# Optimization experiments

Hardware: AMD Instinct MI355X
Metric: run time of the kernel (lower is better)

## Reference

```python
import jax, jax.numpy as jnp
import numpy as np

MIN_, MAX_, KSZ, IGNORE_IDX = 10, 10, 3, -255
B, H, W = 256, 256, 256
LI_MAX_ITERS = 64


def setup_inputs() -> dict:
    key = jax.random.key(0)
    x = jax.random.uniform(key, (B, 1, H, W), dtype=jnp.float32)
    return {"x": x}


def _otsu(hist):
    # hist: [256] counts. Returns Otsu threshold (bin value); fg = img > t.
    bins = jnp.arange(256, dtype=jnp.float32)
    w0 = jnp.cumsum(hist)[:-1]
    w1 = hist.sum() - w0
    s0 = jnp.cumsum(hist * bins)[:-1]
    s_tot = (hist * bins).sum()
    m0 = s0 / jnp.maximum(w0, 1e-12)
    m1 = (s_tot - s0) / jnp.maximum(w1, 1e-12)
    var_b = w0 * w1 * (m0 - m1) ** 2
    return jnp.argmax(var_b).astype(jnp.float32)


def _li(hist, init_t):
    # Histogram-based Li iterative minimum cross-entropy threshold
    # (skimage.filters.threshold_li with initial_guess=init_t).
    bins = jnp.arange(256, dtype=jnp.float32)
    img_min = jnp.min(jnp.where(hist > 0, bins, 255.0))
    vals = bins - img_min  # shift so values >= 0 (as skimage does)
    csum = jnp.cumsum(hist)
    cvsum = jnp.cumsum(hist * vals)
    n_tot, s_tot = csum[-1], cvsum[-1]
    tol = 0.5  # integer image -> half the minimal value spacing

    def body(state):
        t_curr, _, i = state
        # background: img <= t_curr + img_min
        idx = jnp.clip(jnp.floor(t_curr + img_min).astype(jnp.int32), 0, 255)
        n_back, s_back = csum[idx], cvsum[idx]
        n_fore, s_fore = n_tot - n_back, s_tot - s_back
        mean_back = jnp.where(n_back > 0, s_back / jnp.maximum(n_back, 1.0), 0.0)
        mean_fore = s_fore / jnp.maximum(n_fore, 1.0)
        eps = 1e-12
        t_next = (mean_back - mean_fore) / (
            jnp.log(jnp.maximum(mean_back, eps)) - jnp.log(jnp.maximum(mean_fore, eps)))
        t_next = jnp.where(mean_back < eps, mean_fore / 2.0, t_next)
        return (t_next, t_curr, i + 1)

    def cond(state):
        t_curr, t_prev, i = state
        return (jnp.abs(t_curr - t_prev) > tol) & (i < LI_MAX_ITERS)

    t0 = init_t - img_min
    t_fin, _, _ = jax.lax.while_loop(cond, body, (t0, t0 + 10.0, 0))
    return t_fin + img_min


def _sample_mask(key, region, k):
    # Uniform sampling without replacement of up to k pixels from region
    # (bool [H,W]) via random-score top-k (equiv. to torch.multinomial
    # with uniform probs, w/o replacement).
    flat = region.reshape(-1)
    scores = jnp.where(flat, jax.random.uniform(key, (flat.shape[0],)), -1.0)
    top, idx = jax.lax.top_k(scores, k)
    valid = (top >= 0.0).astype(jnp.int32)
    mask = jnp.zeros(flat.shape[0], jnp.int32).at[idx].max(valid)
    return mask.reshape(region.shape)


def _dilate(m):
    # kornia dilation with ones (KSZ,KSZ) kernel on a 0/1 mask == max filter.
    return jax.lax.reduce_window(m, 0, jax.lax.max, (KSZ, KSZ), (1, 1), "SAME")


def _per_image(img_u8, key_fg, key_bg):
    # img_u8: [H,W] int32 in [0,255]
    hist = jnp.zeros(256, jnp.float32).at[img_u8.ravel()].add(1.0)
    otsu = jnp.clip(_otsu(hist), 1.0, 254.0)  # clamp 0->1, 255->254
    li_t = _li(hist, otsu)
    roi = img_u8.astype(jnp.float32) > li_t

    fg = _sample_mask(key_fg, roi, MAX_)
    bg = _sample_mask(key_bg, jnp.logical_not(roi), MIN_)
    if KSZ > 1:
        fg = _dilate(fg)
        bg = _dilate(bg)

    overlap = (fg + bg) == 2
    fg = jnp.where(overlap, 0, fg)
    bg = jnp.where(overlap, 0, bg)

    seeds = jnp.full((H, W), IGNORE_IDX, jnp.int32)
    seeds = jnp.where(bg == 1, 0, seeds)
    seeds = jnp.where(fg == 1, 1, seeds)
    return seeds


def reference(x):
    b = x.shape[0]
    # (cam*255).astype(uint8): truncation, cam in [0,1]
    img = jnp.clip(jnp.floor(x[:, 0] * 255.0), 0, 255).astype(jnp.int32)
    keys = jax.random.split(jax.random.key(1), (b, 2))
    return jax.vmap(_per_image)(img, keys[:, 0], keys[:, 1])
```

## Files before the change

kernel.cpp:

```cpp
#include <hip/hip_runtime.h>
#include <stdint.h>

#define NPIX 65536
#define IGN (-255)
#define CAPB 96

typedef unsigned long long u64;
typedef int v4i __attribute__((ext_vector_type(4)));

__device__ __forceinline__ uint32_t rotl32(uint32_t v, uint32_t r){ return (v<<r)|(v>>(32u-r)); }

__device__ __forceinline__ void tf2x32(uint32_t k0, uint32_t k1, uint32_t x0, uint32_t x1,
                                       uint32_t &o0, uint32_t &o1){
  uint32_t k2 = k0 ^ k1 ^ 0x1BD11BDAu;
  x0 += k0; x1 += k1;
#define TFR(r) { x0 += x1; x1 = rotl32(x1,(r)); x1 ^= x0; }
  TFR(13u) TFR(15u) TFR(26u) TFR(6u)   x0 += k1; x1 += k2 + 1u;
  TFR(17u) TFR(29u) TFR(16u) TFR(24u)  x0 += k2; x1 += k0 + 2u;
  TFR(13u) TFR(15u) TFR(26u) TFR(6u)   x0 += k0; x1 += k1 + 3u;
  TFR(17u) TFR(29u) TFR(16u) TFR(24u)  x0 += k1; x1 += k2 + 4u;
  TFR(13u) TFR(15u) TFR(26u) TFR(6u)   x0 += k2; x1 += k0 + 5u;
#undef TFR
  o0 = x0; o1 = x1;
}

__device__ __forceinline__ uint32_t tf_bits(uint32_t k0, uint32_t k1, uint32_t k2, uint32_t pix){
  uint32_t x0 = k0, x1 = pix + k1;
#define TFR(r) { x0 += x1; x1 = rotl32(x1,(r)); x1 ^= x0; }
  TFR(13u) TFR(15u) TFR(26u) TFR(6u)   x0 += k1; x1 += k2 + 1u;
  TFR(17u) TFR(29u) TFR(16u) TFR(24u)  x0 += k2; x1 += k0 + 2u;
  TFR(13u) TFR(15u) TFR(26u) TFR(6u)   x0 += k0; x1 += k1 + 3u;
  TFR(17u) TFR(29u) TFR(16u) TFR(24u)  x0 += k1; x1 += k2 + 4u;
  TFR(13u) TFR(15u) TFR(26u) TFR(6u)   x0 += k2; x1 += k0 + 5u;
#undef TFR
  return x0 ^ x1;
}

__device__ __forceinline__ u64 packCand(uint32_t bits, uint32_t pix){
  float f = __uint_as_float((bits >> 9) | 0x3f800000u) - 1.0f;
  uint32_t u = __float_as_uint(f) ^ 0x80000000u;
  return ((u64)u << 32) | (u64)(0xFFFFFFFFu - pix);
}

__device__ __forceinline__ void t10_insert(u64* l, u64 c){
  if (c > l[9]) {
    l[9] = c;
#pragma unroll
    for (int i = 9; i > 0; --i){
      u64 a = l[i-1], b2 = l[i];
      if (b2 > a){ l[i-1] = b2; l[i] = a; }
    }
  }
}

__global__ __launch_bounds__(256)
void k1_hist(const float* __restrict__ x, int* __restrict__ out,
             uint32_t* __restrict__ phist, uint32_t* __restrict__ u8c, int use_u8){
  const int img = blockIdx.x >> 3;
  const int chk = blockIdx.x & 7;
  const int tid = threadIdx.x;
  const float4* x4 = (const float4*)(x + (size_t)img * NPIX);
  v4i* o4 = (v4i*)(out + (size_t)img * NPIX);

  __shared__ uint32_t h4[1024];
  h4[tid] = 0u; h4[tid+256] = 0u; h4[tid+512] = 0u; h4[tid+768] = 0u;
  __syncthreads();

  const int sub = tid & 3;
  const v4i f4 = {IGN, IGN, IGN, IGN};
#pragma unroll
  for (int j = 0; j < 8; ++j){
    int p4 = chk*2048 + j*256 + tid;
    float4 v = x4[p4];
    __builtin_nontemporal_store(f4, &o4[p4]);
    uint32_t q0 = (uint32_t)min(max((int)floorf(v.x*255.0f),0),255);
    uint32_t q1 = (uint32_t)min(max((int)floorf(v.y*255.0f),0),255);
    uint32_t q2 = (uint32_t)min(max((int)floorf(v.z*255.0f),0),255);
    uint32_t q3 = (uint32_t)min(max((int)floorf(v.w*255.0f),0),255);
    if (use_u8) u8c[(size_t)img*16384 + p4] = q0 | (q1<<8) | (q2<<16) | (q3<<24);
    atomicAdd(&h4[q0*4+sub],1u); atomicAdd(&h4[q1*4+sub],1u);
    atomicAdd(&h4[q2*4+sub],1u); atomicAdd(&h4[q3*4+sub],1u);
  }
  __syncthreads();
  phist[(size_t)(img*8+chk)*256 + tid] = h4[tid*4] + h4[tid*4+1] + h4[tid*4+2] + h4[tid*4+3];
}

__global__ __launch_bounds__(256)
void k2_score(const float* __restrict__ x, const uint32_t* __restrict__ u8c,
              const uint32_t* __restrict__ phist, uint32_t* __restrict__ qcutp,
              uint32_t* __restrict__ nroip, uint32_t* __restrict__ bcnt,
              u64* __restrict__ cand, int use_u8){
  const int img = blockIdx.x >> 3;
  const int chk = blockIdx.x & 7;
  const int tid = threadIdx.x;

  __shared__ float csum[256], cvsum[256];
  __shared__ u64 s_best;
  __shared__ int s_imin, s_qcut;
  __shared__ uint32_t s_kw[4], s_cnt[2];
  __shared__ u64 s_cand[2][CAPB];

  if (tid < 2){
    uint32_t o0, o1;
    tf2x32(0u, 1u, 0u, (uint32_t)(2*img + tid), o0, o1);
    s_kw[2*tid] = o0; s_kw[2*tid+1] = o1;
  }
  if (tid == 0){ s_imin = 255; s_best = 0ull; s_cnt[0] = 0u; s_cnt[1] = 0u; }

  uint32_t h = 0;
#pragma unroll
  for (int k = 0; k < 8; ++k) h += phist[(size_t)(img*8+k)*256 + tid];
  __syncthreads();
  if (h) atomicMin(&s_imin, tid);
  __syncthreads();
  const float img_min = (float)s_imin;
  csum[tid]  = (float)h;
  cvsum[tid] = (float)h * ((float)tid - img_min);
  __syncthreads();
  for (int off = 1; off < 256; off <<= 1){
    float a = 0.f, c2 = 0.f;
    if (tid >= off){ a = csum[tid-off]; c2 = cvsum[tid-off]; }
    __syncthreads();
    if (tid >= off){ csum[tid] += a; cvsum[tid] += c2; }
    __syncthreads();
  }
  {
    float s_tot_o = cvsum[255] + img_min * csum[255];
    if (tid < 255){
      float w0 = csum[tid], w1 = 65536.0f - w0;
      float cs = cvsum[tid] + img_min * csum[tid];
      float m0 = cs / fmaxf(w0, 1e-12f);
      float m1 = (s_tot_o - cs) / fmaxf(w1, 1e-12f);
      float d = m0 - m1;
      float vb = (w0*w1) * (d*d);
      u64 pk = ((u64)__float_as_uint(vb) << 32) | (u64)(255 - tid);
      atomicMax(&s_best, pk);
    }
  }
  __syncthreads();
  if (tid == 0){
    int bestIdx = 255 - (int)(s_best & 0xFFFFFFFFull);
    float otsu = fminf(fmaxf((float)bestIdx, 1.0f), 254.0f);
    float n_tot = csum[255], s_tot = cvsum[255];
    float t_curr = otsu - img_min, t_prev = t_curr + 10.0f;
    int it = 0;
    while (fabsf(t_curr - t_prev) > 0.5f && it < 64){
      int idx = min(max((int)floorf(t_curr + img_min), 0), 255);
      float n_back = csum[idx], s_back = cvsum[idx];
      float n_fore = n_tot - n_back, s_fore = s_tot - s_back;
      float mean_back = (n_back > 0.0f) ? (s_back / fmaxf(n_back, 1.0f)) : 0.0f;
      float mean_fore = s_fore / fmaxf(n_fore, 1.0f);
      float t_next = (mean_back - mean_fore) /
                     (logf(fmaxf(mean_back, 1e-12f)) - logf(fmaxf(mean_fore, 1e-12f)));
      if (mean_back < 1e-12f) t_next = mean_fore * 0.5f;
      t_prev = t_curr; t_curr = t_next; ++it;
    }
    float lit = t_curr + img_min;
    int qcut = (int)floorf(lit) + 1;
    s_qcut = qcut;
    if (chk == 0){
      uint32_t nroi;
      if (qcut <= 0)        nroi = NPIX;
      else if (qcut > 255)  nroi = 0u;
      else                  nroi = NPIX - (uint32_t)csum[qcut-1];
      qcutp[img] = (uint32_t)qcut;
      nroip[img] = nroi;
    }
  }
  __syncthreads();

  const int qcut = s_qcut;
  const uint32_t fk0 = s_kw[0], fk1 = s_kw[1], bk0 = s_kw[2], bk1 = s_kw[3];
  const uint32_t fk2 = fk0 ^ fk1 ^ 0x1BD11BDAu;
  const uint32_t bk2 = bk0 ^ bk1 ^ 0x1BD11BDAu;
#pragma unroll
  for (int j = 0; j < 8; ++j){
    int p4 = chk*2048 + j*256 + tid;
    uint32_t w;
    if (use_u8){
      w = u8c[(size_t)img*16384 + p4];
    } else {
      float4 v = ((const float4*)(x + (size_t)img*NPIX))[p4];
      uint32_t q0 = (uint32_t)min(max((int)floorf(v.x*255.0f),0),255);
      uint32_t q1 = (uint32_t)min(max((int)floorf(v.y*255.0f),0),255);
      uint32_t q2 = (uint32_t)min(max((int)floorf(v.z*255.0f),0),255);
      uint32_t q3 = (uint32_t)min(max((int)floorf(v.w*255.0f),0),255);
      w = q0 | (q1<<8) | (q2<<16) | (q3<<24);
    }
    uint32_t pix0 = (uint32_t)(p4*4);
#pragma unroll
    for (int s = 0; s < 4; ++s){
      int q = (int)((w >> (8*s)) & 255u);
      bool r = (q >= qcut);
      uint32_t bits = tf_bits(r?fk0:bk0, r?fk1:bk1, r?fk2:bk2, pix0 + (uint32_t)s);
      if (bits >= 0xFF000000u){
        int r2 = r ? 0 : 1;
        uint32_t idx = atomicAdd(&s_cnt[r2], 1u);
        if (idx < CAPB) s_cand[r2][idx] = packCand(bits, pix0 + (uint32_t)s);
      }
    }
  }
  __syncthreads();
  if (tid < 2) bcnt[(size_t)(img*8+chk)*2 + tid] = s_cnt[tid];
  {
    int s = tid >> 7, idx = tid & 127;
    int n = min((int)s_cnt[s], CAPB);
    if (idx < n) cand[((size_t)(img*8+chk)*2 + s)*CAPB + idx] = s_cand[s][idx];
  }
}

__global__ __launch_bounds__(256)
void k3_final(const float* __restrict__ x, int* __restrict__ out,
              const uint32_t* __restrict__ qcutp, const uint32_t* __restrict__ nroip,
              const uint32_t* __restrict__ bcnt, const u64* __restrict__ cand){
  const int img = blockIdx.x;
  const int tid = threadIdx.x;

  __shared__ u64 sbuf[2560];
  __shared__ u64 s_top[2][10];
  __shared__ int s_off[2][9], s_fail[2];
  __shared__ uint32_t s_kw[4];
  __shared__ int s_pr[2][10], s_pc[2][10], s_np[2];

  if (tid < 2){
    uint32_t o0, o1;
    tf2x32(0u, 1u, 0u, (uint32_t)(2*img + tid), o0, o1);
    s_kw[2*tid] = o0; s_kw[2*tid+1] = o1;
  }
  if (tid == 0){
    uint32_t nroi = nroip[img];
    for (int s = 0; s < 2; ++s){
      int off = 0, fail = 0;
      for (int k = 0; k < 8; ++k){
        uint32_t raw = bcnt[(size_t)(img*8+k)*2 + s];
        if (raw > (uint32_t)CAPB) fail = 1;
        int ck = (int)min(raw, (uint32_t)CAPB);
        s_off[s][k] = off; off += ck;
      }
      s_off[s][8] = off;
      int region = s ? (int)(NPIX - nroi) : (int)nroi;
      if (off < 10 && off != region) fail = 1;
      s_fail[s] = fail;
    }
  }
  __syncthreads();

  {
    int s = tid >> 7, idx = tid & 127;
#pragma unroll
    for (int k = 0; k < 8; ++k){
      int ck = s_off[s][k+1] - s_off[s][k];
      if (idx < ck) sbuf[s*1280 + s_off[s][k] + idx] = cand[((size_t)(img*8+k)*2 + s)*CAPB + idx];
    }
  }
  __syncthreads();
  if (tid == 0 || tid == 128){
    int s = tid >> 7;
    if (!s_fail[s]){
      u64 t[10];
#pragma unroll
      for (int i = 0; i < 10; ++i) t[i] = 0ull;
      int n = s_off[s][8];
      for (int i = 0; i < n; ++i) t10_insert(t, sbuf[s*1280 + i]);
#pragma unroll
      for (int i = 0; i < 10; ++i) s_top[s][i] = t[i];
    }
  }
  __syncthreads();

  const int qcut = (int)qcutp[img];
  for (int s = 0; s < 2; ++s){
    if (!s_fail[s]) continue;
    uint32_t kk0 = s_kw[2*s], kk1 = s_kw[2*s+1], kk2 = kk0 ^ kk1 ^ 0x1BD11BDAu;
    u64 t[10];
#pragma unroll
    for (int i = 0; i < 10; ++i) t[i] = 0ull;
    for (int k = 0; k < 256; ++k){
      uint32_t pix = (uint32_t)(tid + 256*k);
      float v = x[(size_t)img*NPIX + pix];
      int q = min(max((int)floorf(v*255.0f),0),255);
      bool r = (q >= qcut);
      if (r == (s == 0)) t10_insert(t, packCand(tf_bits(kk0, kk1, kk2, pix), pix));
    }
#pragma unroll
    for (int i = 0; i < 10; ++i) sbuf[tid*10 + i] = t[i];
    __syncthreads();
    if (tid == 0){
      u64 m[10];
#pragma unroll
      for (int i = 0; i < 10; ++i) m[i] = 0ull;
      for (int i = 0; i < 2560; ++i) t10_insert(m, sbuf[i]);
#pragma unroll
      for (int i = 0; i < 10; ++i) s_top[s][i] = m[i];
    }
    __syncthreads();
  }

  if (tid < 2){
    int np = 0;
    for (int i = 0; i < 10; ++i){
      u64 e = s_top[tid][i];
      if (e){
        uint32_t pix = 0xFFFFFFFFu - (uint32_t)(e & 0xFFFFFFFFull);
        s_pr[tid][np] = (int)(pix >> 8);
        s_pc[tid][np] = (int)(pix & 255u);
        ++np;
      }
    }
    s_np[tid] = np;
  }
  __syncthreads();

  int* outb = out + (size_t)img * NPIX;
  const int nfg = s_np[0], nbg = s_np[1];
  const int npts = nfg + nbg;
  if (tid < npts*9){
    int k = tid / 9, d = tid - k*9;
    int pr = (k < nfg) ? s_pr[0][k] : s_pr[1][k - nfg];
    int pc = (k < nfg) ? s_pc[0][k] : s_pc[1][k - nfg];
    pr += d/3 - 1; pc += d%3 - 1;
    if (pr >= 0 && pr < 256 && pc >= 0 && pc < 256){
      bool fgd = false, bgd = false;
      for (int i = 0; i < nfg; ++i) fgd |= (abs(pr - s_pr[0][i]) <= 1) && (abs(pc - s_pc[0][i]) <= 1);
      for (int i = 0; i < nbg; ++i) bgd |= (abs(pr - s_pr[1][i]) <= 1) && (abs(pc - s_pc[1][i]) <= 1);
      int val = (fgd && bgd) ? IGN : (fgd ? 1 : 0);
      outb[pr*256 + pc] = val;
    }
  }
}

__global__ __launch_bounds__(1024, 4)
void apm_fused(const float* __restrict__ x, int* __restrict__ out){
  const int b = blockIdx.x;
  const int tid = threadIdx.x;
  const float* img = x + (size_t)b * NPIX;
  int* outb = out + (size_t)b * NPIX;

  __shared__ uint32_t hist[256];
  __shared__ float csum[256], cvsum[256];
  __shared__ u64 buf[2][256];
  __shared__ uint32_t s_kw[4];
  __shared__ int s_cnt[2];
  __shared__ int s_nroi, s_imin;
  __shared__ u64 s_best;
  __shared__ float s_lit;
  __shared__ int s_fail[2];
  __shared__ int s_pr[2][10], s_pc[2][10], s_np[2];

  if (tid < 256) hist[tid] = 0u;
  if (tid == 0){ s_cnt[0] = 0; s_cnt[1] = 0; s_nroi = 0; s_imin = 255; s_best = 0ull; }
  if (tid < 2){
    uint32_t o0, o1;
    tf2x32(0u, 1u, 0u, (uint32_t)(2*b + tid), o0, o1);
    s_kw[2*tid] = o0; s_kw[2*tid+1] = o1;
  }
  __syncthreads();

  uint32_t packed[16];
  {
    v4i f4 = {IGN, IGN, IGN, IGN};
    const float4* x4 = (const float4*)img;
    v4i* o4 = (v4i*)outb;
#pragma unroll
    for (int j = 0; j < 16; ++j){
      int p4 = tid + 1024*j;
      float4 v = x4[p4];
      o4[p4] = f4;
      uint32_t u0 = (uint32_t)min(max((int)floorf(v.x*255.0f),0),255);
      uint32_t u1 = (uint32_t)min(max((int)floorf(v.y*255.0f),0),255);
      uint32_t u2 = (uint32_t)min(max((int)floorf(v.z*255.0f),0),255);
      uint32_t u3 = (uint32_t)min(max((int)floorf(v.w*255.0f),0),255);
      packed[j] = u0 | (u1<<8) | (u2<<16) | (u3<<24);
      atomicAdd(&hist[u0],1u); atomicAdd(&hist[u1],1u);
      atomicAdd(&hist[u2],1u); atomicAdd(&hist[u3],1u);
    }
  }
  __syncthreads();
  if (tid < 256 && hist[tid]) atomicMin(&s_imin, tid);
  __syncthreads();
  const float img_min = (float)s_imin;
  if (tid < 256){
    float h = (float)hist[tid];
    csum[tid]  = h;
    cvsum[tid] = h * ((float)tid - img_min);
  }
  __syncthreads();
  for (int off = 1; off < 256; off <<= 1){
    float a = 0.f, c2 = 0.f;
    if (tid < 256 && tid >= off){ a = csum[tid-off]; c2 = cvsum[tid-off]; }
    __syncthreads();
    if (tid < 256 && tid >= off){ csum[tid] += a; cvsum[tid] += c2; }
    __syncthreads();
  }
  {
    float s_tot_o = cvsum[255] + img_min * csum[255];
    if (tid < 255){
      float w0 = csum[tid], w1 = 65536.0f - w0;
      float cs = cvsum[tid] + img_min * csum[tid];
      float m0 = cs / fmaxf(w0, 1e-12f);
      float m1 = (s_tot_o - cs) / fmaxf(w1, 1e-12f);
      float d = m0 - m1;
      float vb = (w0*w1) * (d*d);
      u64 pk = ((u64)__float_as_uint(vb) << 32) | (u64)(255 - tid);
      atomicMax(&s_best, pk);
    }
  }
  __syncthreads();
  if (tid == 0){
    int bestIdx = 255 - (int)(s_best & 0xFFFFFFFFull);
    float otsu = fminf(fmaxf((float)bestIdx, 1.0f), 254.0f);
    float n_tot = csum[255], s_tot = cvsum[255];
    float t_curr = otsu - img_min, t_prev = t_curr + 10.0f;
    int it = 0;
    while (fabsf(t_curr - t_prev) > 0.5f && it < 64){
      int idx = min(max((int)floorf(t_curr + img_min), 0), 255);
      float n_back = csum[idx], s_back = cvsum[idx];
      float n_fore = n_tot - n_back, s_fore = s_tot - s_back;
      float mean_back = (n_back > 0.0f) ? (s_back / fmaxf(n_back, 1.0f)) : 0.0f;
      float mean_fore = s_fore / fmaxf(n_fore, 1.0f);
      float t_next = (mean_back - mean_fore) /
                     (logf(fmaxf(mean_back, 1e-12f)) - logf(fmaxf(mean_fore, 1e-12f)));
      if (mean_back < 1e-12f) t_next = mean_fore * 0.5f;
      t_prev = t_curr; t_curr = t_next; ++it;
    }
    s_lit = t_curr + img_min;
  }
  __syncthreads();

  const float lit = s_lit;
  const uint32_t fk0 = s_kw[0], fk1 = s_kw[1], bk0 = s_kw[2], bk1 = s_kw[3];
  const uint32_t THRM = (0xFF000000u >> 9);
  int my_roi = 0;
#pragma unroll
  for (int j = 0; j < 16; ++j){
    uint32_t pk = packed[j];
    uint32_t pix0 = (uint32_t)(4*(tid + 1024*j));
#pragma unroll
    for (int s = 0; s < 4; ++s){
      uint32_t q = (pk >> (8*s)) & 255u;
      bool r = ((float)q > lit);
      my_roi += r ? 1 : 0;
      uint32_t o0, o1;
      tf2x32(r ? fk0 : bk0, r ? fk1 : bk1, 0u, pix0 + (uint32_t)s, o0, o1);
      uint32_t bits = o0 ^ o1;
      if ((bits >> 9) >= THRM){
        int r2 = r ? 0 : 1;
        int idx = atomicAdd(&s_cnt[r2], 1);
        if (idx < 256) buf[r2][idx] = packCand(bits, pix0 + (uint32_t)s);
      }
    }
  }
  for (int off = 32; off; off >>= 1) my_roi += __shfl_down(my_roi, off);
  if ((tid & 63) == 0) atomicAdd(&s_nroi, my_roi);
  __syncthreads();

  if (tid == 0){
    int m0r = s_nroi, m1r = NPIX - s_nroi;
    int c0 = s_cnt[0], c1 = s_cnt[1];
    s_fail[0] = (c0 > 256) || (c0 < 10 && c0 != m0r);
    s_fail[1] = (c1 > 256) || (c1 < 10 && c1 != m1r);
  }
  __syncthreads();

  if (s_fail[0] || s_fail[1]){
    __shared__ u64 smem[640];
    if (tid < 64){
      for (int r2 = 0; r2 < 2; ++r2){
        if (!s_fail[r2]) continue;
        uint32_t kk0 = s_kw[2*r2], kk1 = s_kw[2*r2+1];
        u64 t[10];
#pragma unroll
        for (int i = 0; i < 10; ++i) t[i] = 0ull;
        for (int k2 = 0; k2 < 1024; ++k2){
          uint32_t pix = (uint32_t)(tid + 64*k2);
          float v = img[pix];
          int q = min(max((int)floorf(v*255.0f),0),255);
          bool r = ((float)q > lit);
          if (r != (r2 == 0)) continue;
          uint32_t o0, o1; tf2x32(kk0, kk1, 0u, pix, o0, o1);
          t10_insert(t, packCand(o0 ^ o1, pix));
        }
#pragma unroll
        for (int i = 0; i < 10; ++i) smem[tid*10 + i] = t[i];
      }
    }
    __syncthreads();
    if (tid < 2 && s_fail[tid]){
      u64 t[10];
#pragma unroll
      for (int i = 0; i < 10; ++i) t[i] = 0ull;
      for (int i = 0; i < 640; ++i) t10_insert(t, smem[i]);
#pragma unroll
      for (int i = 0; i < 10; ++i) buf[tid][i] = t[i];
      s_cnt[tid] = 10;
    }
    __syncthreads();
  }

  if (tid == 0 || tid == 64){
    int r2 = (tid == 0) ? 0 : 1;
    int n = min(s_cnt[r2], 256);
    u64 t[10];
#pragma unroll
    for (int i = 0; i < 10; ++i) t[i] = 0ull;
    for (int i = 0; i < n; ++i) t10_insert(t, buf[r2][i]);
    int np = 0;
    for (int i = 0; i < 10; ++i){
      if (t[i]){
        uint32_t pix = 0xFFFFFFFFu - (uint32_t)(t[i] & 0xFFFFFFFFull);
        s_pr[r2][np] = (int)(pix >> 8);
        s_pc[r2][np] = (int)(pix & 255u);
        ++np;
      }
    }
    s_np[r2] = np;
  }
  __syncthreads();

  const int nfg = s_np[0], nbg = s_np[1];
  const int npts = nfg + nbg;
  if (tid < npts*9){
    int k = tid / 9, d = tid - k*9;
    int pr = (k < nfg) ? s_pr[0][k] : s_pr[1][k - nfg];
    int pc = (k < nfg) ? s_pc[0][k] : s_pc[1][k - nfg];
    pr += d/3 - 1; pc += d%3 - 1;
    if (pr >= 0 && pr < 256 && pc >= 0 && pc < 256){
      bool fgd = false, bgd = false;
      for (int i = 0; i < nfg; ++i) fgd |= (abs(pr - s_pr[0][i]) <= 1) && (abs(pc - s_pc[0][i]) <= 1);
      for (int i = 0; i < nbg; ++i) bgd |= (abs(pr - s_pr[1][i]) <= 1) && (abs(pc - s_pc[1][i]) <= 1);
      int val = (fgd && bgd) ? IGN : (fgd ? 1 : 0);
      outb[pr*256 + pc] = val;
    }
  }
}

extern "C" void kernel_launch(void* const* d_in, const int* in_sizes, int n_in,
                              void* d_out, int out_size, void* d_ws, size_t ws_size,
                              hipStream_t stream) {
  const float* x = (const float*)d_in[0];
  int* out = (int*)d_out;
  int B = in_sizes[0] / NPIX;

  size_t cand_b  = (size_t)B * 8 * 2 * CAPB * 8;
  size_t phist_b = (size_t)B * 8 * 256 * 4;
  size_t qcut_b  = (size_t)B * 4;
  size_t nroi_b  = (size_t)B * 4;
  size_t bcnt_b  = (size_t)B * 8 * 2 * 4;
  size_t base_need = cand_b + phist_b + qcut_b + nroi_b + bcnt_b;
  size_t u8_b = (size_t)B * 16384 * 4;

  if (ws_size < base_need){
    apm_fused<<<B, 1024, 0, stream>>>(x, out);
    return;
  }
  char* p = (char*)d_ws;
  u64*      cand  = (u64*)p;      p += cand_b;
  uint32_t* phist = (uint32_t*)p; p += phist_b;
  uint32_t* qcutp = (uint32_t*)p; p += qcut_b;
  uint32_t* nroip = (uint32_t*)p; p += nroi_b;
  uint32_t* bcnt  = (uint32_t*)p; p += bcnt_b;
  uint32_t* u8c   = (uint32_t*)p;
  int use_u8 = (ws_size >= base_need + u8_b) ? 1 : 0;

  k1_hist <<<B*8, 256, 0, stream>>>(x, out, phist, u8c, use_u8);
  k2_score<<<B*8, 256, 0, stream>>>(x, u8c, phist, qcutp, nroip, bcnt, cand, use_u8);
  k3_final<<<B,   256, 0, stream>>>(x, out, qcutp, nroip, bcnt, cand);
}
```

Before: 200.7 us.

## Split threshold computation into per-image kernel and move output fill to scoring

The Otsu/Li threshold computation, previously repeated redundantly by all 8 chunk blocks of each image in k2_score, now runs once per image in a new k1b_thresh kernel. The -255 output fill moves from k1_hist into k2_score, the u8 cache is made mandatory, and k2_score reads it with 128-bit loads. This removes 8x duplicated serial prefix-scan and Li iteration work, at the cost of an extra kernel launch and a dependency round-trip through global memory.

After: 179.9 us. 10.4% less time.

```diff
diff --git a/kernel.cpp b/kernel.cpp
--- a/kernel.cpp
+++ b/kernel.cpp
@@ -54,30 +54,27 @@
 }
 
 __global__ __launch_bounds__(256)
-void k1_hist(const float* __restrict__ x, int* __restrict__ out,
-             uint32_t* __restrict__ phist, uint32_t* __restrict__ u8c, int use_u8){
+void k1_hist(const float* __restrict__ x, uint32_t* __restrict__ phist,
+             uint32_t* __restrict__ u8c){
   const int img = blockIdx.x >> 3;
   const int chk = blockIdx.x & 7;
   const int tid = threadIdx.x;
   const float4* x4 = (const float4*)(x + (size_t)img * NPIX);
-  v4i* o4 = (v4i*)(out + (size_t)img * NPIX);
 
   __shared__ uint32_t h4[1024];
   h4[tid] = 0u; h4[tid+256] = 0u; h4[tid+512] = 0u; h4[tid+768] = 0u;
   __syncthreads();
 
   const int sub = tid & 3;
-  const v4i f4 = {IGN, IGN, IGN, IGN};
 #pragma unroll
   for (int j = 0; j < 8; ++j){
     int p4 = chk*2048 + j*256 + tid;
     float4 v = x4[p4];
-    __builtin_nontemporal_store(f4, &o4[p4]);
     uint32_t q0 = (uint32_t)min(max((int)floorf(v.x*255.0f),0),255);
     uint32_t q1 = (uint32_t)min(max((int)floorf(v.y*255.0f),0),255);
     uint32_t q2 = (uint32_t)min(max((int)floorf(v.z*255.0f),0),255);
     uint32_t q3 = (uint32_t)min(max((int)floorf(v.w*255.0f),0),255);
-    if (use_u8) u8c[(size_t)img*16384 + p4] = q0 | (q1<<8) | (q2<<16) | (q3<<24);
+    u8c[(size_t)img*16384 + p4] = q0 | (q1<<8) | (q2<<16) | (q3<<24);
     atomicAdd(&h4[q0*4+sub],1u); atomicAdd(&h4[q1*4+sub],1u);
     atomicAdd(&h4[q2*4+sub],1u); atomicAdd(&h4[q3*4+sub],1u);
   }
@@ -86,27 +83,16 @@
 }
 
 __global__ __launch_bounds__(256)
-void k2_score(const float* __restrict__ x, const uint32_t* __restrict__ u8c,
-              const uint32_t* __restrict__ phist, uint32_t* __restrict__ qcutp,
-              uint32_t* __restrict__ nroip, uint32_t* __restrict__ bcnt,
-              u64* __restrict__ cand, int use_u8){
-  const int img = blockIdx.x >> 3;
-  const int chk = blockIdx.x & 7;
+void k1b_thresh(const uint32_t* __restrict__ phist, uint32_t* __restrict__ qcutp,
+                uint32_t* __restrict__ nroip){
+  const int img = blockIdx.x;
   const int tid = threadIdx.x;
 
   __shared__ float csum[256], cvsum[256];
   __shared__ u64 s_best;
-  __shared__ int s_imin, s_qcut;
-  __shared__ uint32_t s_kw[4], s_cnt[2];
-  __shared__ u64 s_cand[2][CAPB];
-
-  if (tid < 2){
-    uint32_t o0, o1;
-    tf2x32(0u, 1u, 0u, (uint32_t)(2*img + tid), o0, o1);
-    s_kw[2*tid] = o0; s_kw[2*tid+1] = o1;
-  }
-  if (tid == 0){ s_imin = 255; s_best = 0ull; s_cnt[0] = 0u; s_cnt[1] = 0u; }
-
+  __shared__ int s_imin;
+
+  if (tid == 0){ s_imin = 255; s_best = 0ull; }
   uint32_t h = 0;
 #pragma unroll
   for (int k = 0; k < 8; ++k) h += phist[(size_t)(img*8+k)*256 + tid];
@@ -157,46 +143,67 @@
     }
     float lit = t_curr + img_min;
     int qcut = (int)floorf(lit) + 1;
-    s_qcut = qcut;
-    if (chk == 0){
-      uint32_t nroi;
-      if (qcut <= 0)        nroi = NPIX;
-      else if (qcut > 255)  nroi = 0u;
-      else                  nroi = NPIX - (uint32_t)csum[qcut-1];
-      qcutp[img] = (uint32_t)qcut;
-      nroip[img] = nroi;
-    }
-  }
-  __syncthreads();
-
-  const int qcut = s_qcut;
+    uint32_t nroi;
+    if (qcut <= 0)        nroi = NPIX;
+    else if (qcut > 255)  nroi = 0u;
+    else                  nroi = NPIX - (uint32_t)csum[qcut-1];
+    qcutp[img] = (uint32_t)qcut;
+    nroip[img] = nroi;
+  }
+}
+
+__global__ __launch_bounds__(256)
+void k2_score(const uint32_t* __restrict__ u8c, int* __restrict__ out,
+              const uint32_t* __restrict__ qcutp, uint32_t* __restrict__ bcnt,
+              u64* __restrict__ cand){
+  const int img = blockIdx.x >> 3;
+  const int chk = blockIdx.x & 7;
+  const int tid = threadIdx.x;
+
+  __shared__ uint32_t s_kw[4], s_cnt[2];
+  __shared__ u64 s_cand[2][CAPB];
+
+  if (tid < 2){
+    uint32_t o0, o1;
+    tf2x32(0u, 1u, 0u, (uint32_t)(2*img + tid), o0, o1);
+    s_kw[2*tid] = o0; s_kw[2*tid+1] = o1;
+  }
+  if (tid == 0){ s_cnt[0] = 0u; s_cnt[1] = 0u; }
+  const int qcut = (int)qcutp[img];
+  __syncthreads();
+
+  {
+    v4i* o4 = (v4i*)(out + (size_t)img * NPIX);
+    const v4i f4 = {IGN, IGN, IGN, IGN};
+#pragma unroll
+    for (int j = 0; j < 8; ++j)
+      __builtin_nontemporal_store(f4, &o4[chk*2048 + j*256 + tid]);
+  }
+
   const uint32_t fk0 = s_kw[0], fk1 = s_kw[1], bk0 = s_kw[2], bk1 = s_kw[3];
   const uint32_t fk2 = fk0 ^ fk1 ^ 0x1BD11BDAu;
   const uint32_t bk2 = bk0 ^ bk1 ^ 0x1BD11BDAu;
-#pragma unroll
-  for (int j = 0; j < 8; ++j){
-    int p4 = chk*2048 + j*256 + tid;
-    uint32_t w;
-    if (use_u8){
-      w = u8c[(size_t)img*16384 + p4];
-    } else {
-      float4 v = ((const float4*)(x + (size_t)img*NPIX))[p4];
-      uint32_t q0 = (uint32_t)min(max((int)floorf(v.x*255.0f),0),255);
-      uint32_t q1 = (uint32_t)min(max((int)floorf(v.y*255.0f),0),255);
-      uint32_t q2 = (uint32_t)min(max((int)floorf(v.z*255.0f),0),255);
-      uint32_t q3 = (uint32_t)min(max((int)floorf(v.w*255.0f),0),255);
-      w = q0 | (q1<<8) | (q2<<16) | (q3<<24);
-    }
-    uint32_t pix0 = (uint32_t)(p4*4);
-#pragma unroll
-    for (int s = 0; s < 4; ++s){
-      int q = (int)((w >> (8*s)) & 255u);
-      bool r = (q >= qcut);
-      uint32_t bits = tf_bits(r?fk0:bk0, r?fk1:bk1, r?fk2:bk2, pix0 + (uint32_t)s);
-      if (bits >= 0xFF000000u){
-        int r2 = r ? 0 : 1;
-        uint32_t idx = atomicAdd(&s_cnt[r2], 1u);
-        if (idx < CAPB) s_cand[r2][idx] = packCand(bits, pix0 + (uint32_t)s);
+  const uint4* u4 = (const uint4*)(u8c + (size_t)img*16384);
+#pragma unroll
+  for (int j = 0; j < 2; ++j){
+    int wi = chk*512 + j*256 + tid;
+    uint4 w4 = u4[wi];
+    uint32_t pix0 = (uint32_t)(wi*16);
+    uint32_t ws4[4] = {w4.x, w4.y, w4.z, w4.w};
+#pragma unroll
+    for (int wsub = 0; wsub < 4; ++wsub){
+      uint32_t w = ws4[wsub];
+#pragma unroll
+      for (int s = 0; s < 4; ++s){
+        int q = (int)((w >> (8*s)) & 255u);
+        bool r = (q >= qcut);
+        uint32_t pix = pix0 + (uint32_t)(wsub*4 + s);
+        uint32_t bits = tf_bits(r?fk0:bk0, r?fk1:bk1, r?fk2:bk2, pix);
+        if (bits >= 0xFF000000u){
+          int r2 = r ? 0 : 1;
+          uint32_t idx = atomicAdd(&s_cnt[r2], 1u);
+          if (idx < CAPB) s_cand[r2][idx] = packCand(bits, pix);
+        }
       }
     }
   }
@@ -546,10 +553,10 @@
   size_t qcut_b  = (size_t)B * 4;
   size_t nroi_b  = (size_t)B * 4;
   size_t bcnt_b  = (size_t)B * 8 * 2 * 4;
-  size_t base_need = cand_b + phist_b + qcut_b + nroi_b + bcnt_b;
-  size_t u8_b = (size_t)B * 16384 * 4;
-
-  if (ws_size < base_need){
+  size_t u8_b    = (size_t)B * 16384 * 4;
+  size_t need = cand_b + phist_b + qcut_b + nroi_b + bcnt_b + u8_b;
+
+  if (ws_size < need){
     apm_fused<<<B, 1024, 0, stream>>>(x, out);
     return;
   }
@@ -560,9 +567,9 @@
   uint32_t* nroip = (uint32_t*)p; p += nroi_b;
   uint32_t* bcnt  = (uint32_t*)p; p += bcnt_b;
   uint32_t* u8c   = (uint32_t*)p;
-  int use_u8 = (ws_size >= base_need + u8_b) ? 1 : 0;
-
-  k1_hist <<<B*8, 256, 0, stream>>>(x, out, phist, u8c, use_u8);
-  k2_score<<<B*8, 256, 0, stream>>>(x, u8c, phist, qcutp, nroip, bcnt, cand, use_u8);
-  k3_final<<<B,   256, 0, stream>>>(x, out, qcutp, nroip, bcnt, cand);
-}
+
+  k1_hist   <<<B*8, 256, 0, stream>>>(x, phist, u8c);
+  k1b_thresh<<<B,   256, 0, stream>>>(phist, qcutp, nroip);
+  k2_score  <<<B*8, 256, 0, stream>>>(u8c, out, qcutp, bcnt, cand);
+  k3_final  <<<B,   256, 0, stream>>>(x, out, qcutp, nroip, bcnt, cand);
+}
```
